# Kernel optimization log

Hardware: AMD Instinct MI355X
Metric: run time of the kernel (lower is better)

The kernel has to match this reference:

```python
import jax, jax.numpy as jnp
import numpy as np

N_EMBED = 384
HEAD_SIZE = 64
B, T = 128, 512


def rope(x):
    # Faithful to source: fres = 1/1000**(arange(0,dim,2)//dim) -> integer
    # floor-div makes the exponent all zeros, so fres == 1 everywhere.
    Bx, Tx, D = x.shape
    half = D // 2
    fres = jnp.ones((half,), dtype=jnp.float32)
    ang = jnp.arange(Tx, dtype=jnp.float32)[:, None] * fres[None, :]  # (T, half)
    cos, sin = jnp.cos(ang), jnp.sin(ang)
    xr = x.reshape(Bx, Tx, half, 2)
    xe, xo = xr[..., 0], xr[..., 1]
    oe = xe * cos - xo * sin
    oo = xe * sin + xo * cos
    return jnp.stack([oe, oo], axis=-1).reshape(Bx, Tx, D)


def setup_inputs() -> dict:
    key = jax.random.key(0)
    ks = jax.random.split(key, 7)
    s = 1.0 / np.sqrt(N_EMBED)
    return {
        "x": jax.random.normal(ks[0], (B, T, N_EMBED), dtype=jnp.float32),
        "wq": jax.random.uniform(ks[1], (N_EMBED, HEAD_SIZE), jnp.float32, -s, s),
        "bq": jax.random.uniform(ks[2], (HEAD_SIZE,), jnp.float32, -s, s),
        "wk": jax.random.uniform(ks[3], (N_EMBED, HEAD_SIZE), jnp.float32, -s, s),
        "bk": jax.random.uniform(ks[4], (HEAD_SIZE,), jnp.float32, -s, s),
        "wv": jax.random.uniform(ks[5], (N_EMBED, HEAD_SIZE), jnp.float32, -s, s),
        "bv": jax.random.uniform(ks[6], (HEAD_SIZE,), jnp.float32, -s, s),
    }


def reference(x, wq, bq, wk, bk, wv, bv):
    Bx, Tx, C = x.shape  # C = n_embed; scale uses C per the source (not head_size)
    q = rope(x @ wq + bq)
    k = rope(x @ wk + bk)
    wei = jnp.einsum("bqd,bkd->bqk", q, k) * (C ** -0.5)  # (B, T, T)
    causal = jnp.tril(jnp.ones((Tx, Tx), dtype=bool))
    wei = jnp.where(causal, wei, -jnp.inf)
    wei = jax.nn.softmax(wei, axis=-1)
    v = x @ wv + bv
    return jnp.einsum("bqk,bkd->bqd", wei, v)
```

## Files before the change

### kernel.cpp

```cpp
#include <hip/hip_runtime.h>

#define TSEQ 512
#define NB   128
#define CDIM 384
#define HD   64
#define QSCALE 0.051031036307982884f
#define MBIAS  8.0f

typedef _Float16 half8  __attribute__((ext_vector_type(8)));
typedef _Float16 half4  __attribute__((ext_vector_type(4)));
typedef float    floatx4 __attribute__((ext_vector_type(4)));

typedef __attribute__((address_space(3))) unsigned int lds_u32;
typedef const __attribute__((address_space(1))) unsigned int g_u32;

__device__ __forceinline__ void load_lds16(const void* g, void* l) {
    __builtin_amdgcn_global_load_lds((g_u32*)g, (lds_u32*)l, 16, 0, 0);
}

__global__ void prep_w(const float* __restrict__ wq, const float* __restrict__ wk,
                       const float* __restrict__ wv, _Float16* __restrict__ Wp)
{
    int i = blockIdx.x * 256 + threadIdx.x;
    if (i >= 3 * CDIM * HD) return;
    int c    = i / 6144;  int r  = i - c * 6144;
    int kblk = r / 1536;  int r2 = r - kblk * 1536;
    int n    = r2 >> 3;   int kin = r2 & 7;
    int k    = c * 32 + kblk * 8 + kin;
    int mat  = n / 64;    int col = n - mat * 64;
    const float* w = (mat == 0) ? wq : ((mat == 1) ? wk : wv);
    Wp[i] = (_Float16)w[k * HD + col];
}

__global__ __launch_bounds__(256) void qkv_gemm(
    const float* __restrict__ x, const _Float16* __restrict__ Wp,
    const float* __restrict__ bq, const float* __restrict__ bk,
    const float* __restrict__ bv,
    _Float16* __restrict__ Qw, _Float16* __restrict__ Kw,
    _Float16* __restrict__ Vtw, int b0)
{
    __shared__ __align__(16) _Float16 wsb[3][6144];

    const int tid  = threadIdx.x;
    const int wave = tid >> 6;
    const int lane = tid & 63;
    const int l16  = lane & 15;
    const int quad = lane >> 4;

    const int row0 = blockIdx.x * 128;
    const size_t rowg = (size_t)b0 * TSEQ + row0;

    int woff[3];
#pragma unroll
    for (int i = 0; i < 3; ++i) woff[i] = (wave * 3 + i) * 512 + lane * 8;

    const float* xp[2];
#pragma unroll
    for (int g = 0; g < 2; ++g)
        xp[g] = x + (rowg + wave * 32 + g * 16 + l16) * CDIM + quad * 8;

    floatx4 acc[2][12];
#pragma unroll
    for (int g = 0; g < 2; ++g)
#pragma unroll
        for (int i = 0; i < 12; ++i)
#pragma unroll
            for (int r = 0; r < 4; ++r) acc[g][i][r] = 0.f;

    floatx4 xA[2][2], xB[2][2];

#define WSTAGE(cc) do { _Pragma("unroll")                                     \
    for (int i_ = 0; i_ < 3; ++i_)                                            \
        load_lds16(Wp + (size_t)(cc) * 6144 + woff[i_],                       \
                   (char*)&wsb[(cc) % 3][0] + (wave * 3 + i_) * 1024);        \
} while (0)

#define XLOAD(cc, S) do { _Pragma("unroll")                                   \
    for (int g_ = 0; g_ < 2; ++g_) {                                          \
        S[g_][0] = *(const floatx4*)(xp[g_] + (cc) * 32);                     \
        S[g_][1] = *(const floatx4*)(xp[g_] + (cc) * 32 + 4);                 \
    }                                                                         \
} while (0)

#define CHUNK(cc, CUR, NXT, VM) do {                                          \
    if ((cc) + 2 < 12) WSTAGE((cc) + 2);                                      \
    if ((cc) + 1 < 12) XLOAD((cc) + 1, NXT);                                  \
    asm volatile("s_waitcnt vmcnt(" VM ")" ::: "memory");                     \
    half8 aF[2];                                                              \
    _Pragma("unroll")                                                         \
    for (int g_ = 0; g_ < 2; ++g_) {                                          \
        _Pragma("unroll")                                                     \
        for (int jj = 0; jj < 8; ++jj)                                        \
            aF[g_][jj] = (_Float16)(jj < 4 ? CUR[g_][0][jj]                   \
                                           : CUR[g_][1][jj - 4]);             \
    }                                                                         \
    const _Float16* bp = &wsb[(cc) % 3][0] + ((size_t)quad * 192 + l16) * 8;  \
    _Pragma("unroll")                                                         \
    for (int i_ = 0; i_ < 12; ++i_) {                                         \
        half8 bb = *(const half8*)(bp + i_ * 128);                            \
        acc[0][i_] = __builtin_amdgcn_mfma_f32_16x16x32_f16(aF[0], bb, acc[0][i_], 0, 0, 0); \
        acc[1][i_] = __builtin_amdgcn_mfma_f32_16x16x32_f16(aF[1], bb, acc[1][i_], 0, 0, 0); \
    }                                                                         \
    __builtin_amdgcn_s_barrier();                                             \
} while (0)

    WSTAGE(0); WSTAGE(1); XLOAD(0, xA);
    asm volatile("s_waitcnt vmcnt(7)" ::: "memory");
    __builtin_amdgcn_s_barrier();

    CHUNK(0,  xA, xB, "7");  CHUNK(1,  xB, xA, "7");
    CHUNK(2,  xA, xB, "7");  CHUNK(3,  xB, xA, "7");
    CHUNK(4,  xA, xB, "7");  CHUNK(5,  xB, xA, "7");
    CHUNK(6,  xA, xB, "7");  CHUNK(7,  xB, xA, "7");
    CHUNK(8,  xA, xB, "7");  CHUNK(9,  xB, xA, "7");
    CHUNK(10, xA, xB, "4");  CHUNK(11, xB, xA, "0");

#undef CHUNK
#undef XLOAD
#undef WSTAGE

    float bq4[4], bk4[4], bv4[4];
#pragma unroll
    for (int s4 = 0; s4 < 4; ++s4) {
        const int cc = s4 * 16 + l16;
        bq4[s4] = bq[cc]; bk4[s4] = bk[cc]; bv4[s4] = bv[cc];
    }
    const int bidx = row0 >> 9;
    const int rb   = wave * 32 + quad * 4;

#pragma unroll
    for (int g = 0; g < 2; ++g) {
        const int t00 = (row0 & (TSEQ - 1)) + rb + g * 16;
        const int r00 = row0 + rb + g * 16;
#pragma unroll
        for (int r = 0; r < 4; ++r) {
            const int t = t00 + r;
            const float st = sinf((float)t);
            const float ct = cosf((float)t);
            const int row = r00 + r;
#pragma unroll
            for (int s4 = 0; s4 < 4; ++s4) {
                const int cc = s4 * 16 + l16;
                float vq = acc[g][s4][r] + bq4[s4];
                float pq = __shfl_xor(vq, 1);
                vq = (cc & 1) ? (pq * st + vq * ct) : (vq * ct - pq * st);
                Qw[(size_t)row * HD + cc] = (_Float16)(vq * QSCALE);
                float vk = acc[g][4 + s4][r] + bk4[s4];
                float pk = __shfl_xor(vk, 1);
                vk = (cc & 1) ? (pk * st + vk * ct) : (vk * ct - pk * st);
                Kw[(size_t)row * HD + cc] = (_Float16)vk;
            }
        }
#pragma unroll
        for (int s4 = 0; s4 < 4; ++s4) {
            const int cc = s4 * 16 + l16;
            half4 vpack;
#pragma unroll
            for (int r = 0; r < 4; ++r)
                vpack[r] = (_Float16)(acc[g][8 + s4][r] + bv4[s4]);
            *(half4*)(Vtw + ((size_t)bidx * HD + cc) * TSEQ + t00) = vpack;
        }
    }
}

__global__ __launch_bounds__(256) void attn_kernel(
    const _Float16* __restrict__ Qw, const _Float16* __restrict__ Kw,
    const _Float16* __restrict__ Vtw, float* __restrict__ out, int b0)
{
    int bx, bl;
    {
        const int lin = blockIdx.y * 8 + blockIdx.x;
        if ((gridDim.y & 7) == 0) {
            const int per = gridDim.y >> 3;
            const int xcd = lin & 7;
            const int k2  = lin >> 3;
            bl = xcd * per + (k2 >> 3);
            bx = k2 & 7;
        } else { bx = blockIdx.x; bl = blockIdx.y; }
    }
    const int tid  = threadIdx.x;
    const int wave = tid >> 6;
    const int lane = tid & 63;
    const int l16  = lane & 15;
    const int quad = lane >> 4;

    const int pr  = bx * 2 + (wave & 1);
    const int h   = wave >> 1;
    const int qA  = pr * 16;
    const int qB  = (31 - pr) * 16;
    const int jdA = pr >> 2;
    const int jdB = (31 - pr) >> 2;

    __shared__ __align__(16) _Float16 pbuf[4][16][72];
    __shared__ __align__(16) floatx4  mbuf[2][10][64];

    const _Float16* Qb = Qw  + (size_t)bl * TSEQ * HD;
    const _Float16* Kb = Kw  + (size_t)bl * TSEQ * HD;
    const _Float16* Vb = Vtw + (size_t)bl * HD * TSEQ;

    half8 aQA0 = *(const half8*)(Qb + (size_t)(qA + l16) * HD + quad * 8);
    half8 aQA1 = *(const half8*)(Qb + (size_t)(qA + l16) * HD + 32 + quad * 8);
    half8 aQB0 = *(const half8*)(Qb + (size_t)(qB + l16) * HD + quad * 8);
    half8 aQB1 = *(const half8*)(Qb + (size_t)(qB + l16) * HD + 32 + quad * 8);

    half8 ones;
#pragma unroll
    for (int jj = 0; jj < 8; ++jj) ones[jj] = (_Float16)1.f;

    floatx4 accO[8], accL[2];
#pragma unroll
    for (int i = 0; i < 8; ++i)
#pragma unroll
        for (int r = 0; r < 4; ++r) accO[i][r] = 0.f;
#pragma unroll
    for (int s = 0; s < 2; ++s)
#pragma unroll
        for (int r = 0; r < 4; ++r) accL[s][r] = 0.f;

    for (int j = h; j <= jdB; j += 2) {
        const int kb = j * 64;

        half8 bK0[4], bK1[4], bV0[4], bV1[4];
#pragma unroll
        for (int s4 = 0; s4 < 4; ++s4) {
            const _Float16* kp = Kb + (size_t)(kb + s4 * 16 + l16) * HD + quad * 8;
            bK0[s4] = *(const half8*)(kp);
            bK1[s4] = *(const half8*)(kp + 32);
            const _Float16* vp = Vb + (size_t)(s4 * 16 + l16) * TSEQ + kb + quad * 8;
            bV0[s4] = *(const half8*)(vp);
            bV1[s4] = *(const half8*)(vp + 32);
        }

        if (j <= jdA) {
            floatx4 st4[4];
            __builtin_amdgcn_s_setprio(1);
#pragma unroll
            for (int s4 = 0; s4 < 4; ++s4) {
#pragma unroll
                for (int r = 0; r < 4; ++r) st4[s4][r] = 0.f;
                st4[s4] = __builtin_amdgcn_mfma_f32_16x16x32_f16(bK0[s4], aQA0, st4[s4], 0, 0, 0);
                st4[s4] = __builtin_amdgcn_mfma_f32_16x16x32_f16(bK1[s4], aQA1, st4[s4], 0, 0, 0);
            }
            __builtin_amdgcn_s_setprio(0);
            const int qrow = qA + l16;
#pragma unroll
            for (int s4 = 0; s4 < 4; ++s4) {
                half4 w;
#pragma unroll
                for (int r = 0; r < 4; ++r) {
                    float p = __expf(fminf(st4[s4][r], 18.f) - MBIAS);
                    if (j == jdA) {
                        const int kcol = kb + s4 * 16 + quad * 4 + r;
                        if (kcol > qrow) p = 0.f;
                    }
                    w[r] = (_Float16)p;
                }
                *(half4*)(&pbuf[wave][l16][s4 * 16 + quad * 4]) = w;
            }
            half8 aP0 = *(const half8*)(&pbuf[wave][l16][quad * 8]);
            half8 aP1 = *(const half8*)(&pbuf[wave][l16][32 + quad * 8]);
            __builtin_amdgcn_s_setprio(1);
#pragma unroll
            for (int s4 = 0; s4 < 4; ++s4) {
                accO[s4] = __builtin_amdgcn_mfma_f32_16x16x32_f16(aP0, bV0[s4], accO[s4], 0, 0, 0);
                accO[s4] = __builtin_amdgcn_mfma_f32_16x16x32_f16(aP1, bV1[s4], accO[s4], 0, 0, 0);
            }
            accL[0] = __builtin_amdgcn_mfma_f32_16x16x32_f16(aP0, ones, accL[0], 0, 0, 0);
            accL[0] = __builtin_amdgcn_mfma_f32_16x16x32_f16(aP1, ones, accL[0], 0, 0, 0);
            __builtin_amdgcn_s_setprio(0);
        }

        {
            floatx4 st4[4];
            __builtin_amdgcn_s_setprio(1);
#pragma unroll
            for (int s4 = 0; s4 < 4; ++s4) {
#pragma unroll
                for (int r = 0; r < 4; ++r) st4[s4][r] = 0.f;
                st4[s4] = __builtin_amdgcn_mfma_f32_16x16x32_f16(bK0[s4], aQB0, st4[s4], 0, 0, 0);
                st4[s4] = __builtin_amdgcn_mfma_f32_16x16x32_f16(bK1[s4], aQB1, st4[s4], 0, 0, 0);
            }
            __builtin_amdgcn_s_setprio(0);
            const int qrow = qB + l16;
#pragma unroll
            for (int s4 = 0; s4 < 4; ++s4) {
                half4 w;
#pragma unroll
                for (int r = 0; r < 4; ++r) {
                    float p = __expf(fminf(st4[s4][r], 18.f) - MBIAS);
                    if (j == jdB) {
                        const int kcol = kb + s4 * 16 + quad * 4 + r;
                        if (kcol > qrow) p = 0.f;
                    }
                    w[r] = (_Float16)p;
                }
                *(half4*)(&pbuf[wave][l16][s4 * 16 + quad * 4]) = w;
            }
            half8 aP0 = *(const half8*)(&pbuf[wave][l16][quad * 8]);
            half8 aP1 = *(const half8*)(&pbuf[wave][l16][32 + quad * 8]);
            __builtin_amdgcn_s_setprio(1);
#pragma unroll
            for (int s4 = 0; s4 < 4; ++s4) {
                accO[4 + s4] = __builtin_amdgcn_mfma_f32_16x16x32_f16(aP0, bV0[s4], accO[4 + s4], 0, 0, 0);
                accO[4 + s4] = __builtin_amdgcn_mfma_f32_16x16x32_f16(aP1, bV1[s4], accO[4 + s4], 0, 0, 0);
            }
            accL[1] = __builtin_amdgcn_mfma_f32_16x16x32_f16(aP0, ones, accL[1], 0, 0, 0);
            accL[1] = __builtin_amdgcn_mfma_f32_16x16x32_f16(aP1, ones, accL[1], 0, 0, 0);
            __builtin_amdgcn_s_setprio(0);
        }
    }

    const int slot = wave & 1;
    if (h == 1) {
#pragma unroll
        for (int i = 0; i < 8; ++i) mbuf[slot][i][lane] = accO[i];
        mbuf[slot][8][lane] = accL[0];
        mbuf[slot][9][lane] = accL[1];
    }
    __syncthreads();
    if (h == 1) return;

#pragma unroll
    for (int i = 0; i < 8; ++i) {
        floatx4 t = mbuf[slot][i][lane];
#pragma unroll
        for (int r = 0; r < 4; ++r) accO[i][r] += t[r];
    }
    {
        floatx4 t8 = mbuf[slot][8][lane];
        floatx4 t9 = mbuf[slot][9][lane];
#pragma unroll
        for (int r = 0; r < 4; ++r) { accL[0][r] += t8[r]; accL[1][r] += t9[r]; }
    }

#pragma unroll
    for (int s = 0; s < 2; ++s) {
        const int qbase = (s == 0) ? qA : qB;
        float inv[4];
#pragma unroll
        for (int r = 0; r < 4; ++r) inv[r] = 1.f / accL[s][r];
#pragma unroll
        for (int s4 = 0; s4 < 4; ++s4) {
            const int dcol = s4 * 16 + l16;
#pragma unroll
            for (int r = 0; r < 4; ++r) {
                const int qr = qbase + quad * 4 + r;
                out[((size_t)(b0 + bl) * TSEQ + qr) * HD + dcol] =
                    accO[s * 4 + s4][r] * inv[r];
            }
        }
    }
}

extern "C" void kernel_launch(void* const* d_in, const int* in_sizes, int n_in,
                              void* d_out, int out_size, void* d_ws, size_t ws_size,
                              hipStream_t stream)
{
    char* ws = (char*)d_ws;
    _Float16* Wp = (_Float16*)ws;
    char* qkv_base = ws + 147456;

    const size_t per_b = (size_t)3 * TSEQ * HD * sizeof(_Float16);
    size_t avail = (ws_size > (size_t)147456) ? ws_size - 147456 : per_b;
    int nbc = (int)(avail / per_b);
    if (nbc > NB) nbc = NB;
    if (nbc < 1)  nbc = 1;

    const size_t chunk_elems = (size_t)nbc * TSEQ * HD;
    _Float16* Qw  = (_Float16*)qkv_base;
    _Float16* Kw  = Qw + chunk_elems;
    _Float16* Vtw = Kw + chunk_elems;

    prep_w<<<dim3((3 * CDIM * HD + 255) / 256), dim3(256), 0, stream>>>(
        (const float*)d_in[1], (const float*)d_in[3], (const float*)d_in[5], Wp);

    for (int b0 = 0; b0 < NB; b0 += nbc) {
        const int nb = (NB - b0 < nbc) ? (NB - b0) : nbc;
        qkv_gemm<<<dim3(nb * 4), dim3(256), 0, stream>>>(
            (const float*)d_in[0], Wp, (const float*)d_in[2], (const float*)d_in[4],
            (const float*)d_in[6], Qw, Kw, Vtw, b0);
        attn_kernel<<<dim3(8, nb), dim3(256), 0, stream>>>(
            Qw, Kw, Vtw, (float*)d_out, b0);
    }
}
```

Baseline: 211.2 us.

## Halve GEMM row tile and split attention key range across four waves

The QKV GEMM block now covers 64 rows instead of 128, so each wave computes one 16-row group and the grid doubles. Occupancy hints are added to both kernels. In the attention kernel each block now handles one query-row pair, with all four waves splitting the key blocks (stride 4), and partial sums are reduced through a three-slot LDS buffer. The V loads are moved after the B-side score MFMAs so they overlap with that compute. This exposes more blocks and parallelism, at the cost of more cross-wave reduction work and redundant Q loads per block.

```diff
diff --git a/kernel.cpp b/kernel.cpp
--- a/kernel.cpp
+++ b/kernel.cpp
@@ -32,7 +32,7 @@
     Wp[i] = (_Float16)w[k * HD + col];
 }
 
-__global__ __launch_bounds__(256) void qkv_gemm(
+__global__ __launch_bounds__(256, 4) void qkv_gemm(
     const float* __restrict__ x, const _Float16* __restrict__ Wp,
     const float* __restrict__ bq, const float* __restrict__ bk,
     const float* __restrict__ bv,
@@ -47,27 +47,22 @@
     const int l16  = lane & 15;
     const int quad = lane >> 4;
 
-    const int row0 = blockIdx.x * 128;
+    const int row0 = blockIdx.x * 64;
     const size_t rowg = (size_t)b0 * TSEQ + row0;
 
     int woff[3];
 #pragma unroll
     for (int i = 0; i < 3; ++i) woff[i] = (wave * 3 + i) * 512 + lane * 8;
 
-    const float* xp[2];
-#pragma unroll
-    for (int g = 0; g < 2; ++g)
-        xp[g] = x + (rowg + wave * 32 + g * 16 + l16) * CDIM + quad * 8;
-
-    floatx4 acc[2][12];
-#pragma unroll
-    for (int g = 0; g < 2; ++g)
-#pragma unroll
-        for (int i = 0; i < 12; ++i)
-#pragma unroll
-            for (int r = 0; r < 4; ++r) acc[g][i][r] = 0.f;
-
-    floatx4 xA[2][2], xB[2][2];
+    const float* xp = x + (rowg + wave * 16 + l16) * CDIM + quad * 8;
+
+    floatx4 acc[12];
+#pragma unroll
+    for (int i = 0; i < 12; ++i)
+#pragma unroll
+        for (int r = 0; r < 4; ++r) acc[i][r] = 0.f;
+
+    floatx4 xA[2], xB[2];
 
 #define WSTAGE(cc) do { _Pragma("unroll")                                     \
     for (int i_ = 0; i_ < 3; ++i_)                                            \
@@ -75,45 +70,38 @@
                    (char*)&wsb[(cc) % 3][0] + (wave * 3 + i_) * 1024);        \
 } while (0)
 
-#define XLOAD(cc, S) do { _Pragma("unroll")                                   \
-    for (int g_ = 0; g_ < 2; ++g_) {                                          \
-        S[g_][0] = *(const floatx4*)(xp[g_] + (cc) * 32);                     \
-        S[g_][1] = *(const floatx4*)(xp[g_] + (cc) * 32 + 4);                 \
-    }                                                                         \
+#define XLOAD(cc, S) do {                                                     \
+    S[0] = *(const floatx4*)(xp + (cc) * 32);                                 \
+    S[1] = *(const floatx4*)(xp + (cc) * 32 + 4);                             \
 } while (0)
 
 #define CHUNK(cc, CUR, NXT, VM) do {                                          \
     if ((cc) + 2 < 12) WSTAGE((cc) + 2);                                      \
     if ((cc) + 1 < 12) XLOAD((cc) + 1, NXT);                                  \
     asm volatile("s_waitcnt vmcnt(" VM ")" ::: "memory");                     \
-    half8 aF[2];                                                              \
+    half8 aF;                                                                 \
     _Pragma("unroll")                                                         \
-    for (int g_ = 0; g_ < 2; ++g_) {                                          \
-        _Pragma("unroll")                                                     \
-        for (int jj = 0; jj < 8; ++jj)                                        \
-            aF[g_][jj] = (_Float16)(jj < 4 ? CUR[g_][0][jj]                   \
-                                           : CUR[g_][1][jj - 4]);             \
-    }                                                                         \
+    for (int jj = 0; jj < 8; ++jj)                                            \
+        aF[jj] = (_Float16)(jj < 4 ? CUR[0][jj] : CUR[1][jj - 4]);            \
     const _Float16* bp = &wsb[(cc) % 3][0] + ((size_t)quad * 192 + l16) * 8;  \
     _Pragma("unroll")                                                         \
     for (int i_ = 0; i_ < 12; ++i_) {                                         \
         half8 bb = *(const half8*)(bp + i_ * 128);                            \
-        acc[0][i_] = __builtin_amdgcn_mfma_f32_16x16x32_f16(aF[0], bb, acc[0][i_], 0, 0, 0); \
-        acc[1][i_] = __builtin_amdgcn_mfma_f32_16x16x32_f16(aF[1], bb, acc[1][i_], 0, 0, 0); \
+        acc[i_] = __builtin_amdgcn_mfma_f32_16x16x32_f16(aF, bb, acc[i_], 0, 0, 0); \
     }                                                                         \
     __builtin_amdgcn_s_barrier();                                             \
 } while (0)
 
     WSTAGE(0); WSTAGE(1); XLOAD(0, xA);
-    asm volatile("s_waitcnt vmcnt(7)" ::: "memory");
+    asm volatile("s_waitcnt vmcnt(5)" ::: "memory");
     __builtin_amdgcn_s_barrier();
 
-    CHUNK(0,  xA, xB, "7");  CHUNK(1,  xB, xA, "7");
-    CHUNK(2,  xA, xB, "7");  CHUNK(3,  xB, xA, "7");
-    CHUNK(4,  xA, xB, "7");  CHUNK(5,  xB, xA, "7");
-    CHUNK(6,  xA, xB, "7");  CHUNK(7,  xB, xA, "7");
-    CHUNK(8,  xA, xB, "7");  CHUNK(9,  xB, xA, "7");
-    CHUNK(10, xA, xB, "4");  CHUNK(11, xB, xA, "0");
+    CHUNK(0,  xA, xB, "5");  CHUNK(1,  xB, xA, "5");
+    CHUNK(2,  xA, xB, "5");  CHUNK(3,  xB, xA, "5");
+    CHUNK(4,  xA, xB, "5");  CHUNK(5,  xB, xA, "5");
+    CHUNK(6,  xA, xB, "5");  CHUNK(7,  xB, xA, "5");
+    CHUNK(8,  xA, xB, "5");  CHUNK(9,  xB, xA, "5");
+    CHUNK(10, xA, xB, "2");  CHUNK(11, xB, xA, "0");
 
 #undef CHUNK
 #undef XLOAD
@@ -126,56 +114,51 @@
         bq4[s4] = bq[cc]; bk4[s4] = bk[cc]; bv4[s4] = bv[cc];
     }
     const int bidx = row0 >> 9;
-    const int rb   = wave * 32 + quad * 4;
-
-#pragma unroll
-    for (int g = 0; g < 2; ++g) {
-        const int t00 = (row0 & (TSEQ - 1)) + rb + g * 16;
-        const int r00 = row0 + rb + g * 16;
-#pragma unroll
-        for (int r = 0; r < 4; ++r) {
-            const int t = t00 + r;
-            const float st = sinf((float)t);
-            const float ct = cosf((float)t);
-            const int row = r00 + r;
-#pragma unroll
-            for (int s4 = 0; s4 < 4; ++s4) {
-                const int cc = s4 * 16 + l16;
-                float vq = acc[g][s4][r] + bq4[s4];
-                float pq = __shfl_xor(vq, 1);
-                vq = (cc & 1) ? (pq * st + vq * ct) : (vq * ct - pq * st);
-                Qw[(size_t)row * HD + cc] = (_Float16)(vq * QSCALE);
-                float vk = acc[g][4 + s4][r] + bk4[s4];
-                float pk = __shfl_xor(vk, 1);
-                vk = (cc & 1) ? (pk * st + vk * ct) : (vk * ct - pk * st);
-                Kw[(size_t)row * HD + cc] = (_Float16)vk;
-            }
-        }
+    const int t00  = (row0 & (TSEQ - 1)) + wave * 16 + quad * 4;
+    const int rowb = row0 + wave * 16 + quad * 4;
+
+#pragma unroll
+    for (int r = 0; r < 4; ++r) {
+        const int t = t00 + r;
+        const float st = sinf((float)t);
+        const float ct = cosf((float)t);
+        const int row = rowb + r;
 #pragma unroll
         for (int s4 = 0; s4 < 4; ++s4) {
             const int cc = s4 * 16 + l16;
-            half4 vpack;
-#pragma unroll
-            for (int r = 0; r < 4; ++r)
-                vpack[r] = (_Float16)(acc[g][8 + s4][r] + bv4[s4]);
-            *(half4*)(Vtw + ((size_t)bidx * HD + cc) * TSEQ + t00) = vpack;
-        }
-    }
-}
-
-__global__ __launch_bounds__(256) void attn_kernel(
+            float vq = acc[s4][r] + bq4[s4];
+            float pq = __shfl_xor(vq, 1);
+            vq = (cc & 1) ? (pq * st + vq * ct) : (vq * ct - pq * st);
+            Qw[(size_t)row * HD + cc] = (_Float16)(vq * QSCALE);
+            float vk = acc[4 + s4][r] + bk4[s4];
+            float pk = __shfl_xor(vk, 1);
+            vk = (cc & 1) ? (pk * st + vk * ct) : (vk * ct - pk * st);
+            Kw[(size_t)row * HD + cc] = (_Float16)vk;
+        }
+    }
+#pragma unroll
+    for (int s4 = 0; s4 < 4; ++s4) {
+        const int cc = s4 * 16 + l16;
+        half4 vpack;
+#pragma unroll
+        for (int r = 0; r < 4; ++r) vpack[r] = (_Float16)(acc[8 + s4][r] + bv4[s4]);
+        *(half4*)(Vtw + ((size_t)bidx * HD + cc) * TSEQ + t00) = vpack;
+    }
+}
+
+__global__ __launch_bounds__(256, 3) void attn_kernel(
     const _Float16* __restrict__ Qw, const _Float16* __restrict__ Kw,
     const _Float16* __restrict__ Vtw, float* __restrict__ out, int b0)
 {
     int bx, bl;
     {
-        const int lin = blockIdx.y * 8 + blockIdx.x;
+        const int lin = blockIdx.y * 16 + blockIdx.x;
         if ((gridDim.y & 7) == 0) {
             const int per = gridDim.y >> 3;
             const int xcd = lin & 7;
             const int k2  = lin >> 3;
-            bl = xcd * per + (k2 >> 3);
-            bx = k2 & 7;
+            bl = xcd * per + (k2 >> 4);
+            bx = k2 & 15;
         } else { bx = blockIdx.x; bl = blockIdx.y; }
     }
     const int tid  = threadIdx.x;
@@ -184,15 +167,15 @@
     const int l16  = lane & 15;
     const int quad = lane >> 4;
 
-    const int pr  = bx * 2 + (wave & 1);
-    const int h   = wave >> 1;
+    const int pr  = bx;
+    const int h   = wave;
     const int qA  = pr * 16;
     const int qB  = (31 - pr) * 16;
     const int jdA = pr >> 2;
     const int jdB = (31 - pr) >> 2;
 
     __shared__ __align__(16) _Float16 pbuf[4][16][72];
-    __shared__ __align__(16) floatx4  mbuf[2][10][64];
+    __shared__ __align__(16) floatx4  mbuf[3][10][64];
 
     const _Float16* Qb = Qw  + (size_t)bl * TSEQ * HD;
     const _Float16* Kb = Kw  + (size_t)bl * TSEQ * HD;
@@ -217,21 +200,19 @@
 #pragma unroll
         for (int r = 0; r < 4; ++r) accL[s][r] = 0.f;
 
-    for (int j = h; j <= jdB; j += 2) {
+    for (int j = h; j <= jdB; j += 4) {
         const int kb = j * 64;
-
-        half8 bK0[4], bK1[4], bV0[4], bV1[4];
+        const bool actA = (j <= jdA);
+
+        half8 bK0[4], bK1[4];
 #pragma unroll
         for (int s4 = 0; s4 < 4; ++s4) {
             const _Float16* kp = Kb + (size_t)(kb + s4 * 16 + l16) * HD + quad * 8;
             bK0[s4] = *(const half8*)(kp);
             bK1[s4] = *(const half8*)(kp + 32);
-            const _Float16* vp = Vb + (size_t)(s4 * 16 + l16) * TSEQ + kb + quad * 8;
-            bV0[s4] = *(const half8*)(vp);
-            bV1[s4] = *(const half8*)(vp + 32);
-        }
-
-        if (j <= jdA) {
+        }
+
+        if (actA) {
             floatx4 st4[4];
             __builtin_amdgcn_s_setprio(1);
 #pragma unroll
@@ -257,6 +238,28 @@
                 }
                 *(half4*)(&pbuf[wave][l16][s4 * 16 + quad * 4]) = w;
             }
+        }
+
+        floatx4 stB[4];
+        __builtin_amdgcn_s_setprio(1);
+#pragma unroll
+        for (int s4 = 0; s4 < 4; ++s4) {
+#pragma unroll
+            for (int r = 0; r < 4; ++r) stB[s4][r] = 0.f;
+            stB[s4] = __builtin_amdgcn_mfma_f32_16x16x32_f16(bK0[s4], aQB0, stB[s4], 0, 0, 0);
+            stB[s4] = __builtin_amdgcn_mfma_f32_16x16x32_f16(bK1[s4], aQB1, stB[s4], 0, 0, 0);
+        }
+        __builtin_amdgcn_s_setprio(0);
+
+        half8 bV0[4], bV1[4];
+#pragma unroll
+        for (int s4 = 0; s4 < 4; ++s4) {
+            const _Float16* vp = Vb + (size_t)(s4 * 16 + l16) * TSEQ + kb + quad * 8;
+            bV0[s4] = *(const half8*)(vp);
+            bV1[s4] = *(const half8*)(vp + 32);
+        }
+
+        if (actA) {
             half8 aP0 = *(const half8*)(&pbuf[wave][l16][quad * 8]);
             half8 aP1 = *(const half8*)(&pbuf[wave][l16][32 + quad * 8]);
             __builtin_amdgcn_s_setprio(1);
@@ -271,23 +274,13 @@
         }
 
         {
-            floatx4 st4[4];
-            __builtin_amdgcn_s_setprio(1);
-#pragma unroll
-            for (int s4 = 0; s4 < 4; ++s4) {
-#pragma unroll
-                for (int r = 0; r < 4; ++r) st4[s4][r] = 0.f;
-                st4[s4] = __builtin_amdgcn_mfma_f32_16x16x32_f16(bK0[s4], aQB0, st4[s4], 0, 0, 0);
-                st4[s4] = __builtin_amdgcn_mfma_f32_16x16x32_f16(bK1[s4], aQB1, st4[s4], 0, 0, 0);
-            }
-            __builtin_amdgcn_s_setprio(0);
             const int qrow = qB + l16;
 #pragma unroll
             for (int s4 = 0; s4 < 4; ++s4) {
                 half4 w;
 #pragma unroll
                 for (int r = 0; r < 4; ++r) {
-                    float p = __expf(fminf(st4[s4][r], 18.f) - MBIAS);
+                    float p = __expf(fminf(stB[s4][r], 18.f) - MBIAS);
                     if (j == jdB) {
                         const int kcol = kb + s4 * 16 + quad * 4 + r;
                         if (kcol > qrow) p = 0.f;
@@ -310,25 +303,25 @@
         }
     }
 
-    const int slot = wave & 1;
-    if (h == 1) {
-#pragma unroll
-        for (int i = 0; i < 8; ++i) mbuf[slot][i][lane] = accO[i];
-        mbuf[slot][8][lane] = accL[0];
-        mbuf[slot][9][lane] = accL[1];
+    if (h != 0) {
+#pragma unroll
+        for (int i = 0; i < 8; ++i) mbuf[h - 1][i][lane] = accO[i];
+        mbuf[h - 1][8][lane] = accL[0];
+        mbuf[h - 1][9][lane] = accL[1];
     }
     __syncthreads();
-    if (h == 1) return;
-
-#pragma unroll
-    for (int i = 0; i < 8; ++i) {
-        floatx4 t = mbuf[slot][i][lane];
-#pragma unroll
-        for (int r = 0; r < 4; ++r) accO[i][r] += t[r];
-    }
-    {
-        floatx4 t8 = mbuf[slot][8][lane];
-        floatx4 t9 = mbuf[slot][9][lane];
+    if (h != 0) return;
+
+#pragma unroll
+    for (int m = 0; m < 3; ++m) {
+#pragma unroll
+        for (int i = 0; i < 8; ++i) {
+            floatx4 t = mbuf[m][i][lane];
+#pragma unroll
+            for (int r = 0; r < 4; ++r) accO[i][r] += t[r];
+        }
+        floatx4 t8 = mbuf[m][8][lane];
+        floatx4 t9 = mbuf[m][9][lane];
 #pragma unroll
         for (int r = 0; r < 4; ++r) { accL[0][r] += t8[r]; accL[1][r] += t9[r]; }
     }
@@ -376,10 +369,10 @@
 
     for (int b0 = 0; b0 < NB; b0 += nbc) {
         const int nb = (NB - b0 < nbc) ? (NB - b0) : nbc;
-        qkv_gemm<<<dim3(nb * 4), dim3(256), 0, stream>>>(
+        qkv_gemm<<<dim3(nb * 8), dim3(256), 0, stream>>>(
             (const float*)d_in[0], Wp, (const float*)d_in[2], (const float*)d_in[4],
             (const float*)d_in[6], Qw, Kw, Vtw, b0);
-        attn_kernel<<<dim3(8, nb), dim3(256), 0, stream>>>(
+        attn_kernel<<<dim3(16, nb), dim3(256), 0, stream>>>(
             Qw, Kw, Vtw, (float*)d_out, b0);
     }
 }
```

New measurement: 207.7 us. Within noise of the previous version (-1.6%).
